# Kernel tuning notes

Measured on AMD Instinct MI355X. Metric: run time of the kernel, lower is better.

The kernel has to match this reference:

```python
import jax, jax.numpy as jnp
import numpy as np

N_NODES = 100000
IN_CH = 128
HID = 64
N_EDGES = 1600000
NEG_SLOPE = 0.2


def setup_inputs() -> dict:
    key = jax.random.key(0)
    k1, k2, k3, k4, k5, k6 = jax.random.split(key, 6)
    x = jax.random.normal(k1, (N_NODES, IN_CH), dtype=jnp.float32)
    edge_index = jax.random.randint(k2, (2, N_EDGES), 0, N_NODES, dtype=jnp.int64)
    # Glorot-style init for GATConv params (heads=1)
    s_w = (2.0 / (IN_CH + HID)) ** 0.5
    W = jax.random.normal(k3, (IN_CH, HID), dtype=jnp.float32) * s_w
    s_a = (2.0 / (1 + HID)) ** 0.5
    att_src = jax.random.normal(k4, (HID,), dtype=jnp.float32) * s_a
    att_dst = jax.random.normal(k5, (HID,), dtype=jnp.float32) * s_a
    bias = jnp.zeros((HID,), dtype=jnp.float32)
    return {"x": x, "edge_index": edge_index, "W": W, "att_src": att_src,
            "att_dst": att_dst, "bias": bias}


def reference(x, edge_index, W, att_src, att_dst, bias):
    N = x.shape[0]
    # PyG GATConv default: add self-loops
    loop = jnp.arange(N, dtype=edge_index.dtype)
    src = jnp.concatenate([edge_index[0], loop])  # message source j
    dst = jnp.concatenate([edge_index[1], loop])  # message target i

    h = x @ W                      # [N, HID]
    a_src = h @ att_src            # [N]
    a_dst = h @ att_dst            # [N]

    # per-edge attention logit: LeakyReLU(a_src[j] + a_dst[i])
    e = jax.nn.leaky_relu(a_src[src] + a_dst[dst], NEG_SLOPE)  # [E+N]
    # numerically-stable segment softmax over destination node
    m = jax.ops.segment_max(e, dst, num_segments=N)
    e = jnp.exp(e - m[dst])
    denom = jax.ops.segment_sum(e, dst, num_segments=N)
    alpha = e / (denom[dst] + 1e-16)               # [E+N]

    # scatter-aggregate weighted source features, then bias
    out = jax.ops.segment_sum(alpha[:, None] * h[src], dst, num_segments=N)
    out = out + bias               # [N, HID]
    return out, alpha[:, None]     # alpha shaped [E+N, heads=1]
```

## Files before the change

kernel.cpp:

```cpp
#include <hip/hip_runtime.h>

#define NN 100000
#define IC 128
#define HD 64
#define NEG 0.2f
#define NPB 32
#define NBKT (NN / NPB)
#define CAP 768
#define NC 196
#define CAP1 9216
#define KB 8
#define CHUNK ((CAP1 + KB - 1) / KB)
#define TILE1 2048
#define NIT1 4

typedef float f32x4 __attribute__((ext_vector_type(4)));
typedef short s16x8 __attribute__((ext_vector_type(8)));

__device__ __forceinline__ unsigned short f32_to_bf16u(float f) {
  union { float f; unsigned int i; } v;
  v.f = f;
  unsigned int b = v.i;
  b += 0x7FFFu + ((b >> 16) & 1u);
  return (unsigned short)(b >> 16);
}

__global__ __launch_bounds__(256) void k_gemm(const float* __restrict__ x,
                                              const float* __restrict__ W,
                                              const float* __restrict__ att_s,
                                              const float* __restrict__ att_d,
                                              unsigned short* __restrict__ hb,
                                              float* __restrict__ as_,
                                              float* __restrict__ ad_,
                                              int* __restrict__ bktcur,
                                              int* __restrict__ ccur) {
  __shared__ unsigned short xb[64 * 128];
  __shared__ unsigned short wt[64 * 128];
  const int tid = threadIdx.x;
  const int n0 = blockIdx.x * 64;
  if (tid < 2 && 2 * blockIdx.x + tid < NBKT) bktcur[2 * blockIdx.x + tid] = 0;
  if (tid == 2 && blockIdx.x < NC) ccur[blockIdx.x] = 0;

  #pragma unroll
  for (int i = 0; i < 8; ++i) {
    int f = i * 256 + tid;
    int r = f >> 5, k0 = (f & 31) << 2;
    float4 v = make_float4(0.f, 0.f, 0.f, 0.f);
    if (n0 + r < NN) v = *(const float4*)&x[(size_t)(n0 + r) * IC + k0];
    ushort4 u;
    u.x = f32_to_bf16u(v.x); u.y = f32_to_bf16u(v.y);
    u.z = f32_to_bf16u(v.z); u.w = f32_to_bf16u(v.w);
    int idx = r * 128 + k0;
    *(ushort4*)&xb[idx ^ ((r & 7) << 3)] = u;
  }
  #pragma unroll
  for (int i = 0; i < 8; ++i) {
    int f = i * 256 + tid;
    int k = f >> 4, c0 = (f & 15) << 2;
    float4 v = *(const float4*)&W[k * HD + c0];
    const float* vf = (const float*)&v;
    #pragma unroll
    for (int j = 0; j < 4; ++j) {
      int c = c0 + j;
      int idx = c * 128 + k;
      wt[idx ^ ((c & 7) << 3)] = f32_to_bf16u(vf[j]);
    }
  }
  __syncthreads();

  const int wv = tid >> 6, lane = tid & 63;
  const int fr = lane & 15;
  const int fq = lane >> 4;
  const int nodeR = wv * 16 + fr;
  f32x4 acc[4] = {};
  #pragma unroll
  for (int kb = 0; kb < 4; ++kb) {
    int ks = kb * 32 + fq * 8;
    int ia = nodeR * 128 + ks;
    s16x8 af = *(s16x8*)&xb[ia ^ ((nodeR & 7) << 3)];
    #pragma unroll
    for (int cg = 0; cg < 4; ++cg) {
      int col = cg * 16 + fr;
      int ib = col * 128 + ks;
      s16x8 bfr = *(s16x8*)&wt[ib ^ ((col & 7) << 3)];
      acc[cg] = __builtin_amdgcn_mfma_f32_16x16x32_bf16(af, bfr, acc[cg], 0, 0, 0);
    }
  }

  float atts[4], attd[4];
  #pragma unroll
  for (int cg = 0; cg < 4; ++cg) {
    atts[cg] = att_s[cg * 16 + fr];
    attd[cg] = att_d[cg * 16 + fr];
  }
  __syncthreads();
  unsigned short* ho = xb;

  #pragma unroll
  for (int j = 0; j < 4; ++j) {
    int nrel = wv * 16 + fq * 4 + j;
    float ps = acc[0][j]*atts[0] + acc[1][j]*atts[1]
             + acc[2][j]*atts[2] + acc[3][j]*atts[3];
    float pd = acc[0][j]*attd[0] + acc[1][j]*attd[1]
             + acc[2][j]*attd[2] + acc[3][j]*attd[3];
    #pragma unroll
    for (int mk = 1; mk < 16; mk <<= 1) {
      ps += __shfl_xor(ps, mk);
      pd += __shfl_xor(pd, mk);
    }
    if (fr == 0 && n0 + nrel < NN) { as_[n0 + nrel] = ps; ad_[n0 + nrel] = pd; }
    #pragma unroll
    for (int cg = 0; cg < 4; ++cg)
      ho[nrel * 72 + cg * 16 + fr] = f32_to_bf16u(acc[cg][j]);
  }
  __syncthreads();

  {
    int node = tid >> 2, ch = (tid & 3) << 4;
    if (n0 + node < NN) {
      ushort4 a0 = *(ushort4*)&ho[node * 72 + ch];
      ushort4 a1 = *(ushort4*)&ho[node * 72 + ch + 4];
      ushort4 a2 = *(ushort4*)&ho[node * 72 + ch + 8];
      ushort4 a3 = *(ushort4*)&ho[node * 72 + ch + 12];
      unsigned short* dst = &hb[(size_t)(n0 + node) * HD + ch];
      *(ushort4*)(dst) = a0;
      *(ushort4*)(dst + 4) = a1;
      *(ushort4*)(dst + 8) = a2;
      *(ushort4*)(dst + 12) = a3;
    }
  }
}

__global__ __launch_bounds__(512) void k_part1(const int* __restrict__ ei,
                                               const float* __restrict__ as_,
                                               const float* __restrict__ ad_,
                                               int* __restrict__ ccur,
                                               unsigned* __restrict__ cbktbuf,
                                               float* __restrict__ p_lin,
                                               int E, int M) {
  __shared__ int lcnt[NC];
  __shared__ int gbs[NC];
  const int tid = threadIdx.x;
  const int base = blockIdx.x * TILE1;

  if (tid < NC) lcnt[tid] = 0;
  __syncthreads();

  unsigned pkx[NIT1];
  int rb[NIT1];
  float tv[NIT1];
  #pragma unroll
  for (int i = 0; i < NIT1; ++i) {
    int m = base + i * 512 + tid;
    if (m < M) {
      int s, d;
      if (m < E) { s = ei[m]; d = ei[E + m]; }
      else       { s = m - E; d = s; }
      int cb = d >> 9;
      pkx[i] = ((unsigned)s << 9) | (d & 511);
      tv[i] = as_[s] + ad_[d];
      int r = atomicAdd(&lcnt[cb], 1);
      rb[i] = (cb << 12) | r;
    } else rb[i] = -1;
  }
  __syncthreads();

  if (tid < NC) {
    int v = lcnt[tid];
    gbs[tid] = v ? atomicAdd(&ccur[tid], v) : 0;
  }
  __syncthreads();

  #pragma unroll
  for (int i = 0; i < NIT1; ++i) {
    if (rb[i] >= 0) {
      int m = base + i * 512 + tid;
      float t = tv[i];
      t = t > 0.f ? t : NEG * t;
      p_lin[m] = __expf(t);
      int cb = (unsigned)rb[i] >> 12, r = rb[i] & 4095;
      int slot = gbs[cb] + r;
      if (slot < CAP1) cbktbuf[(size_t)cb * CAP1 + slot] = pkx[i];
    }
  }
}

__global__ __launch_bounds__(256) void k_part2(const int* __restrict__ ccur,
                                               const unsigned* __restrict__ cbktbuf,
                                               int* __restrict__ bktcur,
                                               unsigned* __restrict__ bktbuf) {
  __shared__ int lcnt[16], gbs[16];
  __shared__ unsigned short rnk[CHUNK];
  __shared__ unsigned pkc[CHUNK];
  const int cb = blockIdx.x >> 3, kb = blockIdx.x & 7;
  const int tid = threadIdx.x;
  const int ccnt = min(ccur[cb], CAP1);
  const int lo = (int)((long)ccnt * kb / KB);
  const int hi = (int)((long)ccnt * (kb + 1) / KB);
  const int len = hi - lo;
  const unsigned* src = cbktbuf + (size_t)cb * CAP1 + lo;

  if (tid < 16) lcnt[tid] = 0;
  __syncthreads();
  for (int i = tid; i < len; i += 256) {
    unsigned u = src[i];
    pkc[i] = u;
    int fb = (u >> 5) & 15;
    int r = atomicAdd(&lcnt[fb], 1);
    rnk[i] = (unsigned short)((fb << 11) | r);
  }
  __syncthreads();
  if (tid < 16) {
    int v = lcnt[tid];
    gbs[tid] = v ? atomicAdd(&bktcur[cb * 16 + tid], v) : 0;
  }
  __syncthreads();
  for (int i = tid; i < len; i += 256) {
    int fb = rnk[i] >> 11, r = rnk[i] & 2047;
    int slot = gbs[fb] + r;
    if (slot < CAP)
      bktbuf[(size_t)(cb * 16 + fb) * CAP + slot] = pkc[i];
  }
}

__global__ __launch_bounds__(256) void k_pg(const int* __restrict__ bktcur,
                                            const unsigned* __restrict__ bktbuf,
                                            const float* __restrict__ as_,
                                            const float* __restrict__ ad_,
                                            const unsigned short* __restrict__ hb,
                                            const float* __restrict__ bias,
                                            float* __restrict__ out,
                                            float* __restrict__ denom) {
  __shared__ int2 sp[CAP];
  __shared__ int cnt2[NPB], nstart[NPB], cur[NPB];
  __shared__ float dls[NPB], adl[NPB];
  const int b = blockIdx.x;
  const int d0 = b << 5;
  const int tid = threadIdx.x;
  const int cnt = min(bktcur[b], CAP);
  const unsigned* mybuf = bktbuf + (size_t)b * CAP;
  const char* hbb = (const char*)hb;

  if (tid < NPB) { cnt2[tid] = 0; adl[tid] = ad_[d0 + tid]; }
  __syncthreads();
  for (int e = tid; e < cnt; e += 256) atomicAdd(&cnt2[mybuf[e] & 31], 1);
  __syncthreads();

  if (tid < 32) {
    int a = cnt2[tid];
    int va = a;
    #pragma unroll
    for (int off = 1; off < 32; off <<= 1) {
      int na = __shfl_up(va, off);
      if (tid >= off) va += na;
    }
    nstart[tid] = va - a;
    cur[tid] = va - a;
  }
  __syncthreads();
  for (int e = tid; e < cnt; e += 256) {
    unsigned v = mybuf[e];
    int node = v & 31;
    float t = as_[v >> 9] + adl[node];
    t = t > 0.f ? t : NEG * t;
    float p = __expf(t);
    int slot = atomicAdd(&cur[node], 1);
    sp[slot] = make_int2((int)((v >> 9) << 7), __float_as_int(p));
  }
  __syncthreads();

  const int wv = tid >> 6, lane = tid & 63;
  const int half = lane >> 5;
  const int hl = lane & 31;
  const unsigned chb = (unsigned)hl << 2;
  const float2 bs2 = *(const float2*)&bias[2 * hl];

  for (int n = wv; n < NPB; n += 4) {
    int beg = nstart[n], end = beg + cnt2[n];
    float ax = 0.f, ay = 0.f, dens = 0.f;
    int e = beg;
    for (; e + 8 <= end; e += 8) {
      #pragma unroll
      for (int j = 0; j < 4; ++j) {
        int2 v = sp[e + 2 * j + half];
        unsigned u = *(const unsigned*)(hbb + ((unsigned)v.x + chb));
        float p = __int_as_float(v.y);
        dens += p;
        ax += p * __uint_as_float(u << 16);
        ay += p * __uint_as_float(u & 0xffff0000u);
      }
    }
    {
      #pragma unroll
      for (int j = 0; j < 4; ++j) {
        int idx = e + 2 * j + half;
        if (idx < end) {
          int2 v = sp[idx];
          unsigned u = *(const unsigned*)(hbb + ((unsigned)v.x + chb));
          float p = __int_as_float(v.y);
          dens += p;
          ax += p * __uint_as_float(u << 16);
          ay += p * __uint_as_float(u & 0xffff0000u);
        }
      }
    }
    ax += __shfl_xor(ax, 32);
    ay += __shfl_xor(ay, 32);
    dens += __shfl_xor(dens, 32);
    if (half == 0) {
      float rd = 1.f / (dens + 1e-16f);
      float2 o;
      o.x = ax * rd + bs2.x;
      o.y = ay * rd + bs2.y;
      *(float2*)&out[(size_t)(d0 + n) * HD + 2 * hl] = o;
      if (hl == 0) dls[n] = dens;
    }
  }
  __syncthreads();
  if (tid < NPB) denom[d0 + tid] = dls[tid];
}

__global__ __launch_bounds__(256) void k_alpha(const int* __restrict__ ei,
                                               const float* __restrict__ p_lin,
                                               const float* __restrict__ denom,
                                               float* __restrict__ alpha_out,
                                               int E, int M) {
  int m = blockIdx.x * 256 + threadIdx.x;
  if (m >= M) return;
  int d = (m < E) ? ei[E + m] : (m - E);
  alpha_out[m] = p_lin[m] / (denom[d] + 1e-16f);
}

extern "C" void kernel_launch(void* const* d_in, const int* in_sizes, int n_in,
                              void* d_out, int out_size, void* d_ws, size_t ws_size,
                              hipStream_t stream) {
  const float* x     = (const float*)d_in[0];
  const int*   ei    = (const int*)d_in[1];
  const float* W     = (const float*)d_in[2];
  const float* att_s = (const float*)d_in[3];
  const float* att_d = (const float*)d_in[4];
  const float* bias  = (const float*)d_in[5];

  const int E = in_sizes[1] / 2;
  const int M = E + NN;

  float* out       = (float*)d_out;
  float* alpha_out = out + (size_t)NN * HD;

  char* w = (char*)d_ws;
  auto alloc = [&](size_t bytes) {
    char* p = w;
    w += (bytes + 15) & ~(size_t)15;
    return p;
  };
  unsigned short* hb = (unsigned short*)alloc(sizeof(unsigned short) * (size_t)NN * HD);
  float*    as_     = (float*)alloc(sizeof(float) * NN);
  float*    ad_     = (float*)alloc(sizeof(float) * NN);
  float*    denom   = (float*)alloc(sizeof(float) * NN);
  float*    p_lin   = (float*)alloc(sizeof(float) * (size_t)M);
  int*      bktcur  = (int*)alloc(sizeof(int) * NBKT);
  int*      ccur    = (int*)alloc(sizeof(int) * NC);
  unsigned* bktbuf  = (unsigned*)alloc(sizeof(unsigned) * (size_t)NBKT * CAP);
  unsigned* cbktbuf = (unsigned*)alloc(sizeof(unsigned) * (size_t)NC * CAP1);

  k_gemm<<<(NN + 63) / 64, 256, 0, stream>>>(x, W, att_s, att_d, hb, as_, ad_,
                                             bktcur, ccur);
  k_part1<<<(M + TILE1 - 1) / TILE1, 512, 0, stream>>>(ei, as_, ad_, ccur,
                                                       cbktbuf, p_lin, E, M);
  k_part2<<<NC * KB, 256, 0, stream>>>(ccur, cbktbuf, bktcur, bktbuf);
  k_pg<<<NBKT, 256, 0, stream>>>(bktcur, bktbuf, as_, ad_, hb, bias, out, denom);
  k_alpha<<<(M + 255) / 256, 256, 0, stream>>>(ei, p_lin, denom, alpha_out,
                                               E, M);
}
```

Measured before the change: 126.9 us.

## Sort edges by destination in second partition pass and recompute alpha logits

The second partition pass now performs a full per-node counting sort inside each 512-node coarse bucket. It writes (source offset, exp logit) pairs contiguously along with per-node begin/end offsets, so the aggregation kernel only copies a contiguous span into LDS and no longer needs its own atomic histogram, scan and scatter. The p_lin buffer is removed: k_alpha recomputes the exp logit from as_/ad_ and the edge indices instead of reading a stored per-edge value. The partition tile size is also doubled. In exchange, each k_part2 block scans its whole coarse bucket twice (two blocks per bucket), and there is extra 8-byte-per-edge traffic through bktbuf2.

```diff
diff --git a/kernel.cpp b/kernel.cpp
--- a/kernel.cpp
+++ b/kernel.cpp
@@ -8,11 +8,10 @@
 #define NBKT (NN / NPB)
 #define CAP 768
 #define NC 196
+#define NPC 512
 #define CAP1 9216
-#define KB 8
-#define CHUNK ((CAP1 + KB - 1) / KB)
-#define TILE1 2048
-#define NIT1 4
+#define TILE1 4096
+#define NIT1 8
 
 typedef float f32x4 __attribute__((ext_vector_type(4)));
 typedef short s16x8 __attribute__((ext_vector_type(8)));
@@ -32,14 +31,12 @@
                                               unsigned short* __restrict__ hb,
                                               float* __restrict__ as_,
                                               float* __restrict__ ad_,
-                                              int* __restrict__ bktcur,
                                               int* __restrict__ ccur) {
   __shared__ unsigned short xb[64 * 128];
   __shared__ unsigned short wt[64 * 128];
   const int tid = threadIdx.x;
   const int n0 = blockIdx.x * 64;
-  if (tid < 2 && 2 * blockIdx.x + tid < NBKT) bktcur[2 * blockIdx.x + tid] = 0;
-  if (tid == 2 && blockIdx.x < NC) ccur[blockIdx.x] = 0;
+  if (tid == 0 && blockIdx.x < NC) ccur[blockIdx.x] = 0;
 
   #pragma unroll
   for (int i = 0; i < 8; ++i) {
@@ -132,11 +129,8 @@
 }
 
 __global__ __launch_bounds__(512) void k_part1(const int* __restrict__ ei,
-                                               const float* __restrict__ as_,
-                                               const float* __restrict__ ad_,
                                                int* __restrict__ ccur,
                                                unsigned* __restrict__ cbktbuf,
-                                               float* __restrict__ p_lin,
                                                int E, int M) {
   __shared__ int lcnt[NC];
   __shared__ int gbs[NC];
@@ -148,7 +142,6 @@
 
   unsigned pkx[NIT1];
   int rb[NIT1];
-  float tv[NIT1];
   #pragma unroll
   for (int i = 0; i < NIT1; ++i) {
     int m = base + i * 512 + tid;
@@ -158,7 +151,6 @@
       else       { s = m - E; d = s; }
       int cb = d >> 9;
       pkx[i] = ((unsigned)s << 9) | (d & 511);
-      tv[i] = as_[s] + ad_[d];
       int r = atomicAdd(&lcnt[cb], 1);
       rb[i] = (cb << 12) | r;
     } else rb[i] = -1;
@@ -174,10 +166,6 @@
   #pragma unroll
   for (int i = 0; i < NIT1; ++i) {
     if (rb[i] >= 0) {
-      int m = base + i * 512 + tid;
-      float t = tv[i];
-      t = t > 0.f ? t : NEG * t;
-      p_lin[m] = __expf(t);
       int cb = (unsigned)rb[i] >> 12, r = rb[i] & 4095;
       int slot = gbs[cb] + r;
       if (slot < CAP1) cbktbuf[(size_t)cb * CAP1 + slot] = pkx[i];
@@ -185,88 +173,98 @@
   }
 }
 
-__global__ __launch_bounds__(256) void k_part2(const int* __restrict__ ccur,
+__global__ __launch_bounds__(512) void k_part2(const int* __restrict__ ccur,
                                                const unsigned* __restrict__ cbktbuf,
-                                               int* __restrict__ bktcur,
-                                               unsigned* __restrict__ bktbuf) {
-  __shared__ int lcnt[16], gbs[16];
-  __shared__ unsigned short rnk[CHUNK];
-  __shared__ unsigned pkc[CHUNK];
-  const int cb = blockIdx.x >> 3, kb = blockIdx.x & 7;
+                                               const float* __restrict__ as_,
+                                               const float* __restrict__ ad_,
+                                               int2* __restrict__ bktbuf2,
+                                               int2* __restrict__ be) {
+  __shared__ int cnt[NPC];
+  __shared__ int start[NPC];
+  __shared__ float adl[NPC];
+  __shared__ unsigned short rnk[CAP1];
+  const int cb = blockIdx.x >> 1, kb = blockIdx.x & 1;
   const int tid = threadIdx.x;
   const int ccnt = min(ccur[cb], CAP1);
-  const int lo = (int)((long)ccnt * kb / KB);
-  const int hi = (int)((long)ccnt * (kb + 1) / KB);
-  const int len = hi - lo;
-  const unsigned* src = cbktbuf + (size_t)cb * CAP1 + lo;
-
-  if (tid < 16) lcnt[tid] = 0;
-  __syncthreads();
-  for (int i = tid; i < len; i += 256) {
+  const unsigned* src = cbktbuf + (size_t)cb * CAP1;
+  const int nlo = kb * 256, nhi = nlo + 256;
+
+  if (tid < NPC) {
+    cnt[tid] = 0;
+    int nd = cb * NPC + tid;
+    adl[tid] = (nd < NN) ? ad_[nd] : 0.f;
+  }
+  __syncthreads();
+
+  for (int i = tid; i < ccnt; i += 512) {
     unsigned u = src[i];
-    pkc[i] = u;
-    int fb = (u >> 5) & 15;
-    int r = atomicAdd(&lcnt[fb], 1);
-    rnk[i] = (unsigned short)((fb << 11) | r);
-  }
-  __syncthreads();
-  if (tid < 16) {
-    int v = lcnt[tid];
-    gbs[tid] = v ? atomicAdd(&bktcur[cb * 16 + tid], v) : 0;
-  }
-  __syncthreads();
-  for (int i = tid; i < len; i += 256) {
-    int fb = rnk[i] >> 11, r = rnk[i] & 2047;
-    int slot = gbs[fb] + r;
-    if (slot < CAP)
-      bktbuf[(size_t)(cb * 16 + fb) * CAP + slot] = pkc[i];
-  }
-}
-
-__global__ __launch_bounds__(256) void k_pg(const int* __restrict__ bktcur,
-                                            const unsigned* __restrict__ bktbuf,
-                                            const float* __restrict__ as_,
-                                            const float* __restrict__ ad_,
+    int r = atomicAdd(&cnt[u & 511], 1);
+    rnk[i] = (unsigned short)r;
+  }
+  __syncthreads();
+
+  if (tid < 64) {
+    int carry = 0;
+    for (int c = 0; c < NPC; c += 64) {
+      int a = cnt[c + tid], v = a;
+      #pragma unroll
+      for (int off = 1; off < 64; off <<= 1) {
+        int nv = __shfl_up(v, off);
+        if (tid >= off) v += nv;
+      }
+      start[c + tid] = carry + v - a;
+      carry += __shfl(v, 63);
+    }
+  }
+  __syncthreads();
+
+  if (tid < 256) {
+    int n = nlo + tid, nd = cb * NPC + n;
+    if (nd < NN)
+      be[nd] = make_int2(cb * CAP1 + start[n], cb * CAP1 + start[n] + cnt[n]);
+  }
+  for (int i = tid; i < ccnt; i += 512) {
+    unsigned u = src[i];
+    int node = u & 511;
+    if (node >= nlo && node < nhi) {
+      int s = u >> 9;
+      float t = as_[s] + adl[node];
+      t = t > 0.f ? t : NEG * t;
+      bktbuf2[(size_t)cb * CAP1 + start[node] + rnk[i]] =
+          make_int2(s << 7, __float_as_int(__expf(t)));
+    }
+  }
+}
+
+__global__ __launch_bounds__(256) void k_pg(const int2* __restrict__ be,
+                                            const int2* __restrict__ bktbuf2,
                                             const unsigned short* __restrict__ hb,
                                             const float* __restrict__ bias,
                                             float* __restrict__ out,
                                             float* __restrict__ denom) {
   __shared__ int2 sp[CAP];
-  __shared__ int cnt2[NPB], nstart[NPB], cur[NPB];
-  __shared__ float dls[NPB], adl[NPB];
+  __shared__ int nsC[NPB], neC[NPB];
+  __shared__ float dls[NPB];
   const int b = blockIdx.x;
   const int d0 = b << 5;
   const int tid = threadIdx.x;
-  const int cnt = min(bktcur[b], CAP);
-  const unsigned* mybuf = bktbuf + (size_t)b * CAP;
   const char* hbb = (const char*)hb;
 
-  if (tid < NPB) { cnt2[tid] = 0; adl[tid] = ad_[d0 + tid]; }
-  __syncthreads();
-  for (int e = tid; e < cnt; e += 256) atomicAdd(&cnt2[mybuf[e] & 31], 1);
-  __syncthreads();
-
-  if (tid < 32) {
-    int a = cnt2[tid];
-    int va = a;
-    #pragma unroll
-    for (int off = 1; off < 32; off <<= 1) {
-      int na = __shfl_up(va, off);
-      if (tid >= off) va += na;
-    }
-    nstart[tid] = va - a;
-    cur[tid] = va - a;
-  }
-  __syncthreads();
-  for (int e = tid; e < cnt; e += 256) {
-    unsigned v = mybuf[e];
-    int node = v & 31;
-    float t = as_[v >> 9] + adl[node];
-    t = t > 0.f ? t : NEG * t;
-    float p = __expf(t);
-    int slot = atomicAdd(&cur[node], 1);
-    sp[slot] = make_int2((int)((v >> 9) << 7), __float_as_int(p));
-  }
+  __shared__ int beg0_s;
+  if (tid < NPB) {
+    int2 r = be[d0 + tid];
+    if (tid == 0) beg0_s = r.x;
+  }
+  __syncthreads();
+  const int beg0 = beg0_s;
+  if (tid < NPB) {
+    int2 r = be[d0 + tid];
+    nsC[tid] = min(r.x - beg0, CAP);
+    neC[tid] = min(r.y - beg0, CAP);
+  }
+  __syncthreads();
+  const int span = neC[NPB - 1];
+  for (int i = tid; i < span; i += 256) sp[i] = bktbuf2[beg0 + i];
   __syncthreads();
 
   const int wv = tid >> 6, lane = tid & 63;
@@ -276,7 +274,7 @@
   const float2 bs2 = *(const float2*)&bias[2 * hl];
 
   for (int n = wv; n < NPB; n += 4) {
-    int beg = nstart[n], end = beg + cnt2[n];
+    int beg = nsC[n], end = neC[n];
     float ax = 0.f, ay = 0.f, dens = 0.f;
     int e = beg;
     for (; e + 8 <= end; e += 8) {
@@ -321,14 +319,19 @@
 }
 
 __global__ __launch_bounds__(256) void k_alpha(const int* __restrict__ ei,
-                                               const float* __restrict__ p_lin,
+                                               const float* __restrict__ as_,
+                                               const float* __restrict__ ad_,
                                                const float* __restrict__ denom,
                                                float* __restrict__ alpha_out,
                                                int E, int M) {
   int m = blockIdx.x * 256 + threadIdx.x;
   if (m >= M) return;
-  int d = (m < E) ? ei[E + m] : (m - E);
-  alpha_out[m] = p_lin[m] / (denom[d] + 1e-16f);
+  int s, d;
+  if (m < E) { s = ei[m]; d = ei[E + m]; }
+  else       { s = m - E; d = s; }
+  float e = as_[s] + ad_[d];
+  e = e > 0.f ? e : NEG * e;
+  alpha_out[m] = __expf(e) / (denom[d] + 1e-16f);
 }
 
 extern "C" void kernel_launch(void* const* d_in, const int* in_sizes, int n_in,
@@ -357,18 +360,16 @@
   float*    as_     = (float*)alloc(sizeof(float) * NN);
   float*    ad_     = (float*)alloc(sizeof(float) * NN);
   float*    denom   = (float*)alloc(sizeof(float) * NN);
-  float*    p_lin   = (float*)alloc(sizeof(float) * (size_t)M);
-  int*      bktcur  = (int*)alloc(sizeof(int) * NBKT);
   int*      ccur    = (int*)alloc(sizeof(int) * NC);
-  unsigned* bktbuf  = (unsigned*)alloc(sizeof(unsigned) * (size_t)NBKT * CAP);
   unsigned* cbktbuf = (unsigned*)alloc(sizeof(unsigned) * (size_t)NC * CAP1);
+  int2*     bktbuf2 = (int2*)alloc(sizeof(int2) * (size_t)NC * CAP1);
+  int2*     be      = (int2*)alloc(sizeof(int2) * (size_t)NN);
 
   k_gemm<<<(NN + 63) / 64, 256, 0, stream>>>(x, W, att_s, att_d, hb, as_, ad_,
-                                             bktcur, ccur);
-  k_part1<<<(M + TILE1 - 1) / TILE1, 512, 0, stream>>>(ei, as_, ad_, ccur,
-                                                       cbktbuf, p_lin, E, M);
-  k_part2<<<NC * KB, 256, 0, stream>>>(ccur, cbktbuf, bktcur, bktbuf);
-  k_pg<<<NBKT, 256, 0, stream>>>(bktcur, bktbuf, as_, ad_, hb, bias, out, denom);
-  k_alpha<<<(M + 255) / 256, 256, 0, stream>>>(ei, p_lin, denom, alpha_out,
+                                             ccur);
+  k_part1<<<(M + TILE1 - 1) / TILE1, 512, 0, stream>>>(ei, ccur, cbktbuf, E, M);
+  k_part2<<<NC * 2, 512, 0, stream>>>(ccur, cbktbuf, as_, ad_, bktbuf2, be);
+  k_pg<<<NBKT, 256, 0, stream>>>(be, bktbuf2, hb, bias, out, denom);
+  k_alpha<<<(M + 255) / 256, 256, 0, stream>>>(ei, as_, ad_, denom, alpha_out,
                                                E, M);
 }
```

After: 131.5 us. +3.6%, slower.
